# Performance work log

Hardware: AMD Instinct MI355X
Metric: run time of the kernel (lower is better)

The kernel has to match this reference:

```python
import jax, jax.numpy as jnp
import numpy as np
from itertools import combinations

NUM_ENT = 7
DIM_ENT = 256
REL_HIDDEN = 256
HIDDEN = 1024
BATCH = 16384
PAIRS = np.array(list(combinations(range(NUM_ENT), 2)), dtype=np.int32)  # [21, 2]


def setup_inputs() -> dict:
    key = jax.random.key(0)
    k1, k2, k3 = jax.random.split(key, 3)
    ctx = jax.random.normal(k1, (BATCH, NUM_ENT * DIM_ENT), dtype=jnp.float32)
    # torch init: uniform(-init_range, init_range) weights, zero bias
    W_rel = jax.random.uniform(k2, (2 * DIM_ENT, REL_HIDDEN), dtype=jnp.float32, minval=-0.01, maxval=0.01)
    b_rel = jnp.zeros((REL_HIDDEN,), dtype=jnp.float32)
    W_fc = jax.random.uniform(k3, (NUM_ENT * DIM_ENT + REL_HIDDEN, HIDDEN), dtype=jnp.float32, minval=-0.01, maxval=0.01)
    b_fc = jnp.zeros((HIDDEN,), dtype=jnp.float32)
    return {"ctx": ctx, "W_rel": W_rel, "b_rel": b_rel, "W_fc": W_fc, "b_fc": b_fc}


def reference(ctx, W_rel, b_rel, W_fc, b_fc):
    B = ctx.shape[0]
    ents = ctx.reshape(B, NUM_ENT, DIM_ENT)
    idx_i = jnp.asarray(PAIRS[:, 0])
    idx_j = jnp.asarray(PAIRS[:, 1])
    # gather both endpoints of each of the 21 pairs: [B, 21, 2*DIM_ENT]
    pair_feat = jnp.concatenate([ents[:, idx_i, :], ents[:, idx_j, :]], axis=-1)
    # batched small Linear + Tanh: [B, 21, REL_HIDDEN]
    rel = jnp.tanh(jnp.einsum("bpe,eh->bph", pair_feat, W_rel) + b_rel)
    # faithful replication of torch: cat pair-major then view(B, rel_hidden, -1).sum(2)
    rel = rel.reshape(B, 21 * REL_HIDDEN).reshape(B, REL_HIDDEN, 21).sum(axis=2)
    inpt = jnp.concatenate([ctx, rel], axis=1)  # [B, input_size]
    # dropout output is discarded in the original forward (no-op); fc1 uses inpt
    out = jnp.tanh(inpt @ W_fc + b_fc)
    return out[None, :, :]  # [1, B, HIDDEN]
```

## Files before the change

### kernel.cpp

```cpp
#include <hip/hip_runtime.h>

typedef unsigned short u16;
typedef __attribute__((ext_vector_type(8))) short short8;
typedef __attribute__((ext_vector_type(4))) float f32x4;
typedef const __attribute__((address_space(1))) unsigned int g_u32;
typedef __attribute__((address_space(3))) unsigned int l_u32;

#define BATCH 16384
#define XCOLS 2048

__device__ __forceinline__ void gload16(const void* g, void* l) {
  __builtin_amdgcn_global_load_lds((g_u32*)g, (l_u32*)l, 16, 0, 0);
}
__device__ __forceinline__ u16 f2bf(float f) {
  unsigned int x = __builtin_bit_cast(unsigned int, f);
  x += 0x7fffu + ((x >> 16) & 1u);
  return (u16)(x >> 16);
}
__device__ __forceinline__ float bf2f(u16 u) {
  return __builtin_bit_cast(float, (unsigned int)u << 16);
}
__device__ __forceinline__ int swz(int P) { return P ^ (((P >> 7) & 7) << 4); }

__device__ __forceinline__ float fast_tanh(float x) {
  float e2 = __expf(2.0f * x);
  return 1.0f - 2.0f * __builtin_amdgcn_rcpf(e2 + 1.0f);
}

__device__ const unsigned char PI[21] = {0,0,0,0,0,0,1,1,1,1,1,2,2,2,2,3,3,3,4,4,5};
__device__ const unsigned char PJ[21] = {1,2,3,4,5,6,2,3,4,5,6,3,4,5,6,4,5,6,5,6,6};

__global__ void prep_ctx(const float* __restrict__ ctx, u16* __restrict__ X) {
  const int total = BATCH * 224;
  for (int u = blockIdx.x * blockDim.x + threadIdx.x; u < total;
       u += gridDim.x * blockDim.x) {
    int b = u / 224, c8 = u - b * 224;
    const float4* s = (const float4*)(ctx + (size_t)b * 1792 + c8 * 8);
    float4 v0 = s[0], v1 = s[1];
    short8 o;
    o[0] = (short)f2bf(v0.x); o[1] = (short)f2bf(v0.y);
    o[2] = (short)f2bf(v0.z); o[3] = (short)f2bf(v0.w);
    o[4] = (short)f2bf(v1.x); o[5] = (short)f2bf(v1.y);
    o[6] = (short)f2bf(v1.z); o[7] = (short)f2bf(v1.w);
    *(short8*)(X + (size_t)b * XCOLS + c8 * 8) = o;
  }
}

__global__ void prep_wrel(const float* __restrict__ Wr, u16* __restrict__ WcT) {
  int idx = blockIdx.x * 256 + threadIdx.x;
  if (idx >= 512 * 256) return;
  int n = idx >> 8, k = idx & 255;
  float v = (n < 256) ? Wr[k * 256 + n] : Wr[(256 + k) * 256 + (n - 256)];
  WcT[idx] = f2bf(v);
}

__global__ void prep_wfc(const float* __restrict__ W, u16* __restrict__ WT) {
  __shared__ float t[64][65];
  int k0 = blockIdx.x * 64;
  int n0 = blockIdx.y * 64;
  int tx = threadIdx.x & 63, ty = threadIdx.x >> 6;
  #pragma unroll
  for (int i = 0; i < 64; i += 4)
    t[ty + i][tx] = W[(size_t)(k0 + ty + i) * 1024 + n0 + tx];
  __syncthreads();
  #pragma unroll
  for (int i = 0; i < 64; i += 4) {
    int n = ty + i;
    WT[(size_t)(n0 + n) * XCOLS + k0 + tx] = f2bf(t[tx][n]);
  }
}

__global__ __launch_bounds__(512, 4) void gemm1_fused(u16* X, const u16* __restrict__ WcT,
                                                      const float* __restrict__ b_rel) {
  __shared__ __align__(16) u16 smem[29184];
  char* sb = (char*)smem;
  const int tid = threadIdx.x;
  const int wid = tid >> 6, lane = tid & 63;
  const int wr = wid >> 2, wc = wid & 3;
  const int b_base = blockIdx.x * 8;
  float* brelL = (float*)(sb + 57344);
  if (tid < 256) brelL[tid] = b_rel[tid];
  f32x4 acc[2][8] = {};
  for (int kt = 0; kt < 8; ++kt) {
    const int kb = kt * 32;
    if (wid < 4) {
      int L = swz((wid * 64 + lane) * 16);
      int row = L >> 6, koff = (L & 63) >> 1;
      int rowc = row < 56 ? row : 0;
      int bl = rowc / 7, e = rowc - bl * 7;
      gload16(X + (size_t)(b_base + bl) * XCOLS + e * 256 + kb + koff, sb + wid * 1024);
    }
    #pragma unroll
    for (int i = 0; i < 4; ++i) {
      int cb = (wid + i * 8) * 64;
      int L = swz((cb + lane) * 16);
      int rn = L >> 6, koff = (L & 63) >> 1;
      gload16(WcT + rn * 256 + kb + koff, sb + 4096 + cb * 16);
    }
    __syncthreads();
    short8 a[2], b[8];
    #pragma unroll
    for (int m = 0; m < 2; ++m) {
      int row = wr * 32 + m * 16 + (lane & 15);
      int L = row * 64 + ((lane >> 4) << 4);
      a[m] = *(const short8*)(sb + swz(L));
    }
    #pragma unroll
    for (int n = 0; n < 8; ++n) {
      int rn = wc * 128 + n * 16 + (lane & 15);
      int L = rn * 64 + ((lane >> 4) << 4);
      b[n] = *(const short8*)(sb + 4096 + swz(L));
    }
    #pragma unroll
    for (int m = 0; m < 2; ++m)
      #pragma unroll
      for (int n = 0; n < 8; ++n)
        acc[m][n] = __builtin_amdgcn_mfma_f32_16x16x32_bf16(a[m], b[n], acc[m][n], 0, 0, 0);
    __syncthreads();
  }
  #pragma unroll
  for (int m = 0; m < 2; ++m) {
    int row0 = wr * 32 + m * 16 + ((lane >> 4) << 2);
    #pragma unroll
    for (int n = 0; n < 8; ++n) {
      int col = wc * 128 + n * 16 + (lane & 15);
      #pragma unroll
      for (int v = 0; v < 4; ++v) {
        int row = row0 + v;
        if (row < 56) {
          int L = row * 1024 + col * 2;
          *(u16*)(sb + (L ^ ((row & 7) << 4))) = f2bf(acc[m][n][v]);
        }
      }
    }
  }
  __syncthreads();
  #pragma unroll
  for (int i = 0; i < 4; ++i) {
    int o = tid + i * 512;
    int bl = o >> 8, r = o & 255;
    float sum = 0.f;
    #pragma unroll
    for (int c = 0; c < 21; ++c) {
      int k = r * 21 + c;
      int p = k >> 8, h = k & 255;
      int ri = bl * 7 + PI[p], rj = bl * 7 + PJ[p];
      int Lu = ri * 1024 + h * 2;
      int Lv = rj * 1024 + 512 + h * 2;
      float uv = bf2f(*(const u16*)(sb + (Lu ^ ((ri & 7) << 4))));
      float vv = bf2f(*(const u16*)(sb + (Lv ^ ((rj & 7) << 4))));
      sum += fast_tanh(uv + vv + brelL[h]);
    }
    X[(size_t)(b_base + bl) * XCOLS + 1792 + r] = f2bf(sum);
  }
}

__global__ __launch_bounds__(256, 3) void gemm2(const u16* __restrict__ X, const u16* __restrict__ WT,
                                                const float* __restrict__ b_fc, float* __restrict__ out) {
  __shared__ __align__(16) u16 smem[16384];
  char* sb = (char*)smem;
  const int tid = threadIdx.x;
  const int wid = tid >> 6, lane = tid & 63;
  const int wr = wid >> 1, wc = wid & 1;
  int bid = blockIdx.x;
  int sw = (bid & 7) * 128 + (bid >> 3);
  int bm = sw >> 3, bn = sw & 7;
  const size_t mBase = (size_t)bm * 128;
  const int nBase = bn * 128;
  f32x4 acc[4][4] = {};
  for (int kt = 0; kt < 32; ++kt) {
    const int kb = kt * 64;
    #pragma unroll
    for (int i = 0; i < 4; ++i) {
      int cb = (wid + i * 4) * 64;
      int L = swz((cb + lane) * 16);
      int row = L >> 7, koff = (L & 127) >> 1;
      gload16(X + (mBase + row) * XCOLS + kb + koff, sb + cb * 16);
      gload16(WT + (size_t)(nBase + row) * XCOLS + kb + koff, sb + 16384 + cb * 16);
    }
    __syncthreads();
    #pragma unroll
    for (int kk = 0; kk < 64; kk += 32) {
      short8 a[4], b[4];
      #pragma unroll
      for (int m = 0; m < 4; ++m) {
        int row = wr * 64 + m * 16 + (lane & 15);
        int L = row * 128 + kk * 2 + ((lane >> 4) << 4);
        a[m] = *(const short8*)(sb + swz(L));
      }
      #pragma unroll
      for (int n = 0; n < 4; ++n) {
        int rn = wc * 64 + n * 16 + (lane & 15);
        int L = rn * 128 + kk * 2 + ((lane >> 4) << 4);
        b[n] = *(const short8*)(sb + 16384 + swz(L));
      }
      #pragma unroll
      for (int m = 0; m < 4; ++m)
        #pragma unroll
        for (int n = 0; n < 4; ++n)
          acc[m][n] = __builtin_amdgcn_mfma_f32_16x16x32_bf16(a[m], b[n], acc[m][n], 0, 0, 0);
    }
    __syncthreads();
  }
  #pragma unroll
  for (int m = 0; m < 4; ++m) {
    int row0 = wr * 64 + m * 16 + ((lane >> 4) << 2);
    #pragma unroll
    for (int n = 0; n < 4; ++n) {
      int col = nBase + wc * 64 + n * 16 + (lane & 15);
      float bias = b_fc[col];
      #pragma unroll
      for (int v = 0; v < 4; ++v)
        out[(mBase + row0 + v) * 1024 + col] = fast_tanh(acc[m][n][v] + bias);
    }
  }
}

extern "C" void kernel_launch(void* const* d_in, const int* in_sizes, int n_in,
                              void* d_out, int out_size, void* d_ws, size_t ws_size,
                              hipStream_t stream) {
  const float* ctx   = (const float*)d_in[0];
  const float* W_rel = (const float*)d_in[1];
  const float* b_rel = (const float*)d_in[2];
  const float* W_fc  = (const float*)d_in[3];
  const float* b_fc  = (const float*)d_in[4];
  float* out = (float*)d_out;
  u16* X    = (u16*)d_ws;
  u16* WcT  = X + (size_t)BATCH * XCOLS;
  u16* WfcT = WcT + 512 * 256;
  prep_ctx<<<2048, 256, 0, stream>>>(ctx, X);
  prep_wrel<<<512, 256, 0, stream>>>(W_rel, WcT);
  prep_wfc<<<dim3(32, 16), 256, 0, stream>>>(W_fc, WfcT);
  gemm1_fused<<<2048, 512, 0, stream>>>(X, WcT, b_rel);
  gemm2<<<1024, 256, 0, stream>>>(X, WfcT, b_fc, out);
}
```

Measured before the change: 223.5 us.

## Restructure rel GEMM tiling and vectorize tanh-sum epilogue in rounds

```diff
diff --git a/kernel.cpp b/kernel.cpp
--- a/kernel.cpp
+++ b/kernel.cpp
@@ -70,88 +70,105 @@
   }
 }
 
-__global__ __launch_bounds__(512, 4) void gemm1_fused(u16* X, const u16* __restrict__ WcT,
+__global__ __launch_bounds__(512, 4) void gemm1_fused(u16* __restrict__ X, const u16* __restrict__ WcT,
                                                       const float* __restrict__ b_rel) {
-  __shared__ __align__(16) u16 smem[29184];
+  __shared__ __align__(16) u16 smem[36864];
   char* sb = (char*)smem;
   const int tid = threadIdx.x;
   const int wid = tid >> 6, lane = tid & 63;
-  const int wr = wid >> 2, wc = wid & 3;
   const int b_base = blockIdx.x * 8;
-  float* brelL = (float*)(sb + 57344);
-  if (tid < 256) brelL[tid] = b_rel[tid];
-  f32x4 acc[2][8] = {};
-  for (int kt = 0; kt < 8; ++kt) {
-    const int kb = kt * 32;
-    if (wid < 4) {
-      int L = swz((wid * 64 + lane) * 16);
-      int row = L >> 6, koff = (L & 63) >> 1;
-      int rowc = row < 56 ? row : 0;
-      int bl = rowc / 7, e = rowc - bl * 7;
+  float brl[4];
+  #pragma unroll
+  for (int n = 0; n < 4; ++n)
+    brl[n] = 0.5f * b_rel[(wid & 3) * 64 + n * 16 + (lane & 15)];
+  f32x4 acc[4][4] = {};
+  for (int kt = 0; kt < 4; ++kt) {
+    const int kb = kt * 64;
+    {
+      int L = swz(tid * 16);
+      int row = L >> 7, koff = (L & 127) >> 1;
+      int r = row < 56 ? row : 55;
+      int bl = r / 7, e = r - bl * 7;
       gload16(X + (size_t)(b_base + bl) * XCOLS + e * 256 + kb + koff, sb + wid * 1024);
     }
     #pragma unroll
-    for (int i = 0; i < 4; ++i) {
-      int cb = (wid + i * 8) * 64;
-      int L = swz((cb + lane) * 16);
-      int rn = L >> 6, koff = (L & 63) >> 1;
-      gload16(WcT + rn * 256 + kb + koff, sb + 4096 + cb * 16);
-    }
-    __syncthreads();
-    short8 a[2], b[8];
-    #pragma unroll
-    for (int m = 0; m < 2; ++m) {
-      int row = wr * 32 + m * 16 + (lane & 15);
-      int L = row * 64 + ((lane >> 4) << 4);
-      a[m] = *(const short8*)(sb + swz(L));
-    }
-    #pragma unroll
-    for (int n = 0; n < 8; ++n) {
-      int rn = wc * 128 + n * 16 + (lane & 15);
-      int L = rn * 64 + ((lane >> 4) << 4);
-      b[n] = *(const short8*)(sb + 4096 + swz(L));
-    }
-    #pragma unroll
-    for (int m = 0; m < 2; ++m)
-      #pragma unroll
-      for (int n = 0; n < 8; ++n)
-        acc[m][n] = __builtin_amdgcn_mfma_f32_16x16x32_bf16(a[m], b[n], acc[m][n], 0, 0, 0);
-    __syncthreads();
-  }
-  #pragma unroll
-  for (int m = 0; m < 2; ++m) {
-    int row0 = wr * 32 + m * 16 + ((lane >> 4) << 2);
-    #pragma unroll
-    for (int n = 0; n < 8; ++n) {
-      int col = wc * 128 + n * 16 + (lane & 15);
+    for (int i = 0; i < 8; ++i) {
+      int slot = i * 512 + tid;
+      int L = swz(slot * 16);
+      int rn = L >> 7, koff = (L & 127) >> 1;
+      gload16(WcT + rn * 256 + kb + koff, sb + 8192 + (i * 512 + wid * 64) * 16);
+    }
+    __syncthreads();
+    #pragma unroll
+    for (int kk = 0; kk < 64; kk += 32) {
+      short8 a[4], b[4];
+      #pragma unroll
+      for (int m = 0; m < 4; ++m) {
+        int row = m * 16 + (lane & 15);
+        int L = row * 128 + kk * 2 + ((lane >> 4) << 4);
+        a[m] = *(const short8*)(sb + swz(L));
+      }
+      #pragma unroll
+      for (int n = 0; n < 4; ++n) {
+        int rn = wid * 64 + n * 16 + (lane & 15);
+        int L = rn * 128 + kk * 2 + ((lane >> 4) << 4);
+        b[n] = *(const short8*)(sb + 8192 + swz(L));
+      }
+      #pragma unroll
+      for (int m = 0; m < 4; ++m)
+        #pragma unroll
+        for (int n = 0; n < 4; ++n)
+          acc[m][n] = __builtin_amdgcn_mfma_f32_16x16x32_bf16(a[m], b[n], acc[m][n], 0, 0, 0);
+    }
+    __syncthreads();
+  }
+  for (int rd = 0; rd < 4; ++rd) {
+    const int rbase = rd * 14;
+    #pragma unroll
+    for (int m = 0; m < 4; ++m) {
+      int row0 = m * 16 + ((lane >> 4) << 2);
       #pragma unroll
       for (int v = 0; v < 4; ++v) {
-        int row = row0 + v;
-        if (row < 56) {
-          int L = row * 1024 + col * 2;
-          *(u16*)(sb + (L ^ ((row & 7) << 4))) = f2bf(acc[m][n][v]);
+        int lr = row0 + v - rbase;
+        if (lr >= 0 && lr < 14) {
+          #pragma unroll
+          for (int n = 0; n < 4; ++n) {
+            int col = wid * 64 + n * 16 + (lane & 15);
+            int L = lr * 1024 + col * 2;
+            *(u16*)(sb + (L ^ ((lr & 7) << 4))) = f2bf(acc[m][n][v] + brl[n]);
+          }
         }
       }
     }
-  }
-  __syncthreads();
-  #pragma unroll
-  for (int i = 0; i < 4; ++i) {
-    int o = tid + i * 512;
-    int bl = o >> 8, r = o & 255;
-    float sum = 0.f;
-    #pragma unroll
-    for (int c = 0; c < 21; ++c) {
-      int k = r * 21 + c;
-      int p = k >> 8, h = k & 255;
-      int ri = bl * 7 + PI[p], rj = bl * 7 + PJ[p];
-      int Lu = ri * 1024 + h * 2;
-      int Lv = rj * 1024 + 512 + h * 2;
-      float uv = bf2f(*(const u16*)(sb + (Lu ^ ((ri & 7) << 4))));
-      float vv = bf2f(*(const u16*)(sb + (Lv ^ ((rj & 7) << 4))));
-      sum += fast_tanh(uv + vv + brelL[h]);
-    }
-    X[(size_t)(b_base + bl) * XCOLS + 1792 + r] = f2bf(sum);
+    __syncthreads();
+    for (int i = tid; i < 1344; i += 512) {
+      int bb = i >= 672;
+      int rem = i - bb * 672;
+      int k8 = rem * 8;
+      int p = k8 >> 8, h = k8 & 255;
+      int li = bb * 7 + PI[p], lj = bb * 7 + PJ[p];
+      int Lu = li * 1024 + h * 2;
+      int Lv = lj * 1024 + 512 + h * 2;
+      short8 uu = *(const short8*)(sb + (Lu ^ ((li & 7) << 4)));
+      short8 vv = *(const short8*)(sb + (Lv ^ ((lj & 7) << 4)));
+      float t[8];
+      #pragma unroll
+      for (int e = 0; e < 8; ++e)
+        t[e] = fast_tanh(bf2f((u16)uu[e]) + bf2f((u16)vv[e]));
+      f32x4* T = (f32x4*)(sb + 14336 + bb * 21504 + k8 * 4);
+      T[0] = f32x4{t[0], t[1], t[2], t[3]};
+      T[1] = f32x4{t[4], t[5], t[6], t[7]};
+    }
+    __syncthreads();
+    {
+      int bb = tid >> 8, r = tid & 255;
+      const float* T = (const float*)(sb + 14336 + bb * 21504);
+      float s = 0.f;
+      #pragma unroll
+      for (int c = 0; c < 21; ++c) s += T[r * 21 + c];
+      X[(size_t)(b_base + rd * 2 + bb) * XCOLS + 1792 + r] = f2bf(s);
+    }
+    __syncthreads();
   }
 }
 
```

After: 201.4 us. 1.11x faster.
